# Kernel optimization log

Hardware: AMD Instinct MI355X
Metric: run time of the kernel (lower is better)

Reference implementation:

```python
import jax, jax.numpy as jnp
import numpy as np

B, H, OH, C, T = 512, 1024, 4096, 512, 40


def setup_inputs() -> dict:
    key = jax.random.key(0)
    ks = jax.random.split(key, 5)
    scaled = lambda k, sh, fan: (jax.random.normal(k, sh, jnp.float32) / np.sqrt(fan).astype(np.float32))
    return dict(
        z=jax.random.normal(ks[0], (B, H), jnp.float32),
        timestamps=jnp.arange(T, dtype=jnp.float32) * 0.1,  # spacing == rk4 step_size
        W1=scaled(ks[1], (H, OH), H), b1=jnp.zeros((OH,), jnp.float32),
        W2=scaled(ks[2], (OH, H), OH), b2=jnp.zeros((H,), jnp.float32),
        Wf=scaled(ks[3], (H, C), H), bf=jnp.zeros((C,), jnp.float32),
    )


def reference(z, timestamps, W1, b1, W2, b2, Wf, bf):
    # odefunc: autonomous neural-ODE MLP f(y) = tanh(y W1 + b1) W2 + b2
    def f(y):
        return jnp.tanh(y @ W1 + b1) @ W2 + b2

    # torchdiffeq 'rk4' = 3/8-rule RK4 (rk4_alt_step_func); one step per
    # timestamp interval since spacing == step_size == 0.1
    def step(y, ts):
        t0, t1 = ts
        dt = t1 - t0
        k1 = f(y)
        k2 = f(y + dt * k1 / 3.0)
        k3 = f(y + dt * (k2 - k1 / 3.0))
        k4 = f(y + dt * (k1 - k2 + k3))
        y_new = y + dt * (k1 + 3.0 * (k2 + k3) + k4) / 8.0
        return y_new, y_new

    _, ys = jax.lax.scan(step, z, (timestamps[:-1], timestamps[1:]))
    pred_z = jnp.concatenate([z[None], ys], axis=0)  # [T, B, H], includes y0
    return jax.nn.softmax(pred_z @ Wf + bf, axis=-1)  # [T, B, C]
```

## Files before the change

### kernel.cpp

```cpp
#include <hip/hip_runtime.h>
#include <hip/hip_bf16.h>
#include <math.h>

using bf16 = __hip_bfloat16;
typedef __bf16 bf16x8 __attribute__((ext_vector_type(8)));
typedef float f32x4 __attribute__((ext_vector_type(4)));

static constexpr int NB = 512, NH = 1024, NOH = 4096, NC = 512, NT = 40;
static constexpr int SPLITK = 4;
static constexpr int NCNT = 128;

#define AL(p) __hip_atomic_load((p), __ATOMIC_RELAXED, __HIP_MEMORY_SCOPE_AGENT)
#define ASF(p, v) __hip_atomic_store((p), (v), __ATOMIC_RELAXED, __HIP_MEMORY_SCOPE_AGENT)
#define AFA(p, v) __hip_atomic_fetch_add((p), (v), __ATOMIC_RELAXED, __HIP_MEMORY_SCOPE_AGENT)

__device__ __forceinline__ float lo32f(unsigned long long v) {
  return __uint_as_float((unsigned)v);
}
__device__ __forceinline__ float hi32f(unsigned long long v) {
  return __uint_as_float((unsigned)(v >> 32));
}


__global__ void transpose_cast(const float* __restrict__ W, bf16* __restrict__ WT,
                               int K, int N) {
  __shared__ float tile[32][33];
  const int n0 = blockIdx.x * 32;
  const int k0 = blockIdx.y * 32;
  const int tx = threadIdx.x;
  const int ty = threadIdx.y;
#pragma unroll
  for (int i = 0; i < 4; ++i) {
    int r = ty + i * 8;
    tile[r][tx] = W[(size_t)(k0 + r) * N + n0 + tx];
  }
  __syncthreads();
#pragma unroll
  for (int i = 0; i < 4; ++i) {
    int r = ty + i * 8;
    const int n = n0 + r, k = k0 + tx;
    WT[(size_t)n * K + (k ^ ((n & 7) << 3))] = __float2bfloat16(tile[tx][r]);
  }
}

__global__ void init_state(const float* __restrict__ z, float* __restrict__ y,
                           bf16* __restrict__ yb, bf16* __restrict__ pred0,
                           unsigned* __restrict__ cnt) {
  const int i = blockIdx.x * 256 + threadIdx.x;
  const int r = i >> 10, c = i & (NH - 1);
  float v = z[i];
  y[i] = v;
  bf16 b = __float2bfloat16(v);
  const int sw = r * NH + (c ^ ((r & 7) << 3));
  yb[sw] = b;
  pred0[sw] = b;
  if (i < (NT - 1) * 4 * NCNT) cnt[i] = 0u;
}

template <int EPI>
__global__ __launch_bounds__(256, 3) void gemm_stage(
    const bf16* __restrict__ A, const bf16* __restrict__ BT,
    const float* __restrict__ bias, bf16* __restrict__ outB,
    float* __restrict__ part, float* __restrict__ y, bf16* __restrict__ yb,
    float* __restrict__ k1, float* __restrict__ k2, float* __restrict__ k3,
    bf16* __restrict__ pred_next, const float* __restrict__ ts, int t, int s,
    unsigned* __restrict__ cnt) {
  constexpr int BK = 64;
  constexpr int KCH = 1024;
  constexpr int KST = (EPI == 0) ? NH : NOH;
  constexpr int NOUT = (EPI == 0) ? NOH : NH;
  constexpr int NI = KCH / BK;

  __shared__ __align__(16) bf16 As[3][64 * BK];
  __shared__ __align__(16) bf16 Bs[3][64 * BK];

  const int tid = threadIdx.x;
  const int lane = tid & 63;
  const int wave = tid >> 6;
  const int wr = wave >> 1, wc = wave & 1;
  const int l15 = lane & 15, kg = lane >> 4;
  const int xorB = (l15 & 7) << 4;
  const int srow = tid >> 3;
  const int scol = (tid & 7) * 8;

  const int bid = blockIdx.x;
  const int xcd = bid & 7, slot = bid >> 3;
  int row0, col0, kbeg, kz = 0, strip = 0, rb = 0;
  if constexpr (EPI == 0) {
    col0 = (xcd + ((slot & 7) << 3)) * 64;
    row0 = (slot >> 3) * 64;
    kbeg = 0;
  } else {
    strip = xcd + ((slot & 1) << 3);
    col0 = strip * 64;
    kz = (slot >> 1) & 3;
    rb = slot >> 3;
    row0 = rb * 64;
    kbeg = kz * KCH;
  }

  f32x4 acc[2][2] = {};

  auto stage = [&](int buf, int kt) {
#pragma unroll
    for (int i = 0; i < 2; ++i) {
      const bf16* ga = A + (size_t)(row0 + i * 32 + srow) * KST + kt + scol;
      __builtin_amdgcn_global_load_lds(
          (const __attribute__((address_space(1))) void*)ga,
          (__attribute__((address_space(3))) void*)&As[buf][i * 2048 + tid * 8],
          16, 0, 0);
      const bf16* gb = BT + (size_t)(col0 + i * 32 + srow) * KST + kt + scol;
      __builtin_amdgcn_global_load_lds(
          (const __attribute__((address_space(1))) void*)gb,
          (__attribute__((address_space(3))) void*)&Bs[buf][i * 2048 + tid * 8],
          16, 0, 0);
    }
  };

  stage(0, kbeg);
  stage(1, kbeg + BK);
  int cur = 0, nxt = 2;

#pragma unroll 1
  for (int j = 0; j < NI; ++j) {
    if (j < NI - 1) asm volatile("s_waitcnt vmcnt(4)" ::: "memory");
    else            asm volatile("s_waitcnt vmcnt(0)" ::: "memory");
    __builtin_amdgcn_s_barrier();
    __builtin_amdgcn_sched_barrier(0);
    if (j + 2 < NI) stage(nxt, kbeg + (j + 2) * BK);
    __builtin_amdgcn_sched_barrier(0);

    const char* Ab = (const char*)&As[cur][0];
    const char* Bb = (const char*)&Bs[cur][0];
#pragma unroll
    for (int ks = 0; ks < BK; ks += 32) {
      const int kb2 = (ks + kg * 8) * 2;
      bf16x8 af[2], bf_[2];
#pragma unroll
      for (int mi = 0; mi < 2; ++mi) {
        const int r = wr * 32 + mi * 16 + l15;
        af[mi] = *reinterpret_cast<const bf16x8*>(Ab + ((r * 128 + kb2) ^ xorB));
      }
#pragma unroll
      for (int ni = 0; ni < 2; ++ni) {
        const int r = wc * 32 + ni * 16 + l15;
        bf_[ni] = *reinterpret_cast<const bf16x8*>(Bb + ((r * 128 + kb2) ^ xorB));
      }
#pragma unroll
      for (int mi = 0; mi < 2; ++mi)
#pragma unroll
        for (int ni = 0; ni < 2; ++ni)
          acc[mi][ni] = __builtin_amdgcn_mfma_f32_16x16x32_bf16(
              af[mi], bf_[ni], acc[mi][ni], 0, 0, 0);
    }
    cur = (cur == 2) ? 0 : cur + 1;
    nxt = (nxt == 2) ? 0 : nxt + 1;
  }

  if constexpr (EPI == 0) {
#pragma unroll
    for (int mi = 0; mi < 2; ++mi) {
      const int gr0 = row0 + wr * 32 + mi * 16 + kg * 4;
#pragma unroll
      for (int ni = 0; ni < 2; ++ni) {
        const int gcol = col0 + wc * 32 + ni * 16 + l15;
        const float b = bias[gcol];
#pragma unroll
        for (int j = 0; j < 4; ++j) {
          const int r = gr0 + j;
          outB[(size_t)r * NOUT + (gcol ^ ((r & 7) << 3))] =
              __float2bfloat16(tanhf(acc[mi][ni][j] + b));
        }
      }
    }
  } else {
    float* pz = part + (size_t)kz * (NB * NH);
#pragma unroll
    for (int mi = 0; mi < 2; ++mi) {
      const int gr0 = row0 + wr * 32 + mi * 16 + kg * 4;
#pragma unroll
      for (int ni = 0; ni < 2; ++ni) {
        const int gcol = col0 + wc * 32 + ni * 16 + l15;
#pragma unroll
        for (int j = 0; j < 4; ++j)
          ASF(&pz[(size_t)(gr0 + j) * NH + gcol], acc[mi][ni][j]);
      }
    }
    __syncthreads();
    __shared__ unsigned arrS;
    if (tid == 0) arrS = AFA(&cnt[rb * 16 + strip], 1u);
    __syncthreads();
    if (arrS == (unsigned)(SPLITK - 1)) {
      const float dtv = ts[t + 1] - ts[t];
#pragma unroll
      for (int q = 0; q < 4; ++q) {
        const int v = q * 256 + tid;
        const int r = v >> 4, c4 = v & 15;
        const int row = row0 + r, col = col0 + c4 * 4;
        const size_t gi = (size_t)row * NH + col;
        f32x4 sum = {};
#pragma unroll
        for (int z = 0; z < SPLITK; ++z) {
          const unsigned long long* pp =
              (const unsigned long long*)(part + (size_t)z * (NB * NH) + gi);
          unsigned long long u0 = AL(pp), u1 = AL(pp + 1);
          sum[0] += lo32f(u0); sum[1] += hi32f(u0);
          sum[2] += lo32f(u1); sum[3] += hi32f(u1);
        }
        const f32x4 bb = *reinterpret_cast<const f32x4*>(bias + col);
        const f32x4 ksv = sum + bb;
        const f32x4 yv = *reinterpret_cast<const f32x4*>(y + gi);
        f32x4 yn;
        if (s == 1) {
          *reinterpret_cast<f32x4*>(k1 + gi) = ksv;
          yn = yv + ksv * (dtv / 3.0f);
        } else if (s == 2) {
          const f32x4 k1v = *reinterpret_cast<const f32x4*>(k1 + gi);
          *reinterpret_cast<f32x4*>(k2 + gi) = ksv;
          yn = yv + (ksv - k1v * (1.0f / 3.0f)) * dtv;
        } else if (s == 3) {
          const f32x4 k1v = *reinterpret_cast<const f32x4*>(k1 + gi);
          const f32x4 k2v = *reinterpret_cast<const f32x4*>(k2 + gi);
          *reinterpret_cast<f32x4*>(k3 + gi) = ksv;
          yn = yv + (k1v - k2v + ksv) * dtv;
        } else {
          const f32x4 k1v = *reinterpret_cast<const f32x4*>(k1 + gi);
          const f32x4 k2v = *reinterpret_cast<const f32x4*>(k2 + gi);
          const f32x4 k3v = *reinterpret_cast<const f32x4*>(k3 + gi);
          yn = yv + (k1v + (k2v + k3v) * 3.0f + ksv) * (dtv * 0.125f);
          *reinterpret_cast<f32x4*>(y + gi) = yn;
        }
        union { bf16 h4[4]; unsigned long long u; } pk;
#pragma unroll
        for (int j = 0; j < 4; ++j) pk.h4[j] = __float2bfloat16(yn[j]);
        const size_t sw =
            (size_t)row * NH + (((col & ~7) ^ ((row & 7) << 3)) | (col & 7));
        *reinterpret_cast<unsigned long long*>(yb + sw) = pk.u;
        if (s == 4)
          *reinterpret_cast<unsigned long long*>(pred_next + sw) = pk.u;
      }
    }
  }
}

__global__ __launch_bounds__(256, 1) void proj_gemm(
    const bf16* __restrict__ A, const bf16* __restrict__ BT,
    int M, int N, int K, const float* __restrict__ bias,
    float* __restrict__ outF) {
  __shared__ __align__(16) bf16 As[2][128 * 64];
  __shared__ __align__(16) bf16 Bs[2][128 * 64];

  const int tid = threadIdx.x;
  const int lane = tid & 63;
  const int wave = tid >> 6;
  const int wr = wave >> 1, wc = wave & 1;
  const int row0 = blockIdx.y * 128, col0 = blockIdx.x * 128;
  const int l15 = lane & 15, kg = lane >> 4;
  const int xorB = (l15 & 7) << 4;
  const int srow = tid >> 3;
  const int scol = (tid & 7) * 8;

  f32x4 acc[4][4] = {};

  auto stage = [&](int buf, int kt) {
#pragma unroll
    for (int i = 0; i < 4; ++i) {
      const bf16* ga = A + (size_t)(row0 + i * 32 + srow) * K + kt + scol;
      __builtin_amdgcn_global_load_lds(
          (const __attribute__((address_space(1))) void*)ga,
          (__attribute__((address_space(3))) void*)&As[buf][i * 2048 + tid * 8],
          16, 0, 0);
      const bf16* gb = BT + (size_t)(col0 + i * 32 + srow) * K + kt + scol;
      __builtin_amdgcn_global_load_lds(
          (const __attribute__((address_space(1))) void*)gb,
          (__attribute__((address_space(3))) void*)&Bs[buf][i * 2048 + tid * 8],
          16, 0, 0);
    }
  };

  stage(0, 0);
  __syncthreads();
  int cur = 0;

  for (int kt = 0; kt < K; kt += 64) {
    if (kt + 64 < K) stage(cur ^ 1, kt + 64);
#pragma unroll
    for (int ks = 0; ks < 64; ks += 32) {
      const int kb2 = (ks + kg * 8) * 2;
      bf16x8 af[4], bf_[4];
#pragma unroll
      for (int mi = 0; mi < 4; ++mi) {
        const int r = wr * 64 + mi * 16 + l15;
        af[mi] = *reinterpret_cast<const bf16x8*>(
            (const char*)&As[cur][0] + ((r * 128 + kb2) ^ xorB));
      }
#pragma unroll
      for (int ni = 0; ni < 4; ++ni) {
        const int r = wc * 64 + ni * 16 + l15;
        bf_[ni] = *reinterpret_cast<const bf16x8*>(
            (const char*)&Bs[cur][0] + ((r * 128 + kb2) ^ xorB));
      }
#pragma unroll
      for (int mi = 0; mi < 4; ++mi)
#pragma unroll
        for (int ni = 0; ni < 4; ++ni)
          acc[mi][ni] = __builtin_amdgcn_mfma_f32_16x16x32_bf16(
              af[mi], bf_[ni], acc[mi][ni], 0, 0, 0);
    }
    __syncthreads();
    cur ^= 1;
  }

#pragma unroll
  for (int mi = 0; mi < 4; ++mi) {
    const int gr0 = row0 + wr * 64 + mi * 16 + kg * 4;
#pragma unroll
    for (int ni = 0; ni < 4; ++ni) {
      const int gcol = col0 + wc * 64 + ni * 16 + l15;
      const float b = bias[gcol];
#pragma unroll
      for (int j = 0; j < 4; ++j)
        outF[(size_t)(gr0 + j) * N + gcol] = acc[mi][ni][j] + b;
    }
  }
}

__global__ void softmax_rows(float* __restrict__ out) {
  const int row = blockIdx.x * 4 + (threadIdx.x >> 6);
  const int lane = threadIdx.x & 63;
  float* p = out + (size_t)row * NC + lane * 8;
  f32x4 a = *reinterpret_cast<const f32x4*>(p);
  f32x4 b = *reinterpret_cast<const f32x4*>(p + 4);

  float m = fmaxf(fmaxf(fmaxf(a[0], a[1]), fmaxf(a[2], a[3])),
                  fmaxf(fmaxf(b[0], b[1]), fmaxf(b[2], b[3])));
#pragma unroll
  for (int off = 32; off > 0; off >>= 1) m = fmaxf(m, __shfl_xor(m, off));

  f32x4 ea, eb;
  float sum = 0.0f;
#pragma unroll
  for (int j = 0; j < 4; ++j) { ea[j] = expf(a[j] - m); sum += ea[j]; }
#pragma unroll
  for (int j = 0; j < 4; ++j) { eb[j] = expf(b[j] - m); sum += eb[j]; }
#pragma unroll
  for (int off = 32; off > 0; off >>= 1) sum += __shfl_xor(sum, off);

  const float inv = 1.0f / sum;
  ea *= inv;
  eb *= inv;
  *reinterpret_cast<f32x4*>(p) = ea;
  *reinterpret_cast<f32x4*>(p + 4) = eb;
}

extern "C" void kernel_launch(void* const* d_in, const int* in_sizes, int n_in,
                              void* d_out, int out_size, void* d_ws, size_t ws_size,
                              hipStream_t stream) {
  const float* z = (const float*)d_in[0];
  const float* ts = (const float*)d_in[1];
  const float* W1 = (const float*)d_in[2];
  const float* b1 = (const float*)d_in[3];
  const float* W2 = (const float*)d_in[4];
  const float* b2 = (const float*)d_in[5];
  const float* Wf = (const float*)d_in[6];
  const float* bfv = (const float*)d_in[7];

  char* w = (char*)d_ws;
  bf16* W1bT = (bf16*)w;          w += (size_t)NOH * NH * 2;
  bf16* W2bT = (bf16*)w;          w += (size_t)NH * NOH * 2;
  bf16* WfT  = (bf16*)w;          w += (size_t)NC * NH * 2;
  float* y   = (float*)w;         w += (size_t)NB * NH * 4;
  bf16* yb   = (bf16*)w;          w += (size_t)NB * NH * 2;
  float* k1  = (float*)w;         w += (size_t)NB * NH * 4;
  float* k2  = (float*)w;         w += (size_t)NB * NH * 4;
  float* k3  = (float*)w;         w += (size_t)NB * NH * 4;
  bf16* h    = (bf16*)w;          w += (size_t)NB * NOH * 2;
  float* part = (float*)w;        w += (size_t)SPLITK * NB * NH * 4;
  bf16* pred = (bf16*)w;          w += (size_t)NT * NB * NH * 2;
  unsigned* cnt = (unsigned*)w;   w += (size_t)(NT - 1) * 4 * NCNT * 4;

  float* logits = (float*)d_out;

  transpose_cast<<<dim3(NOH / 32, NH / 32), dim3(32, 8), 0, stream>>>(W1, W1bT, NH, NOH);
  transpose_cast<<<dim3(NH / 32, NOH / 32), dim3(32, 8), 0, stream>>>(W2, W2bT, NOH, NH);
  transpose_cast<<<dim3(NC / 32, NH / 32), dim3(32, 8), 0, stream>>>(Wf, WfT, NH, NC);
  init_state<<<(NB * NH) / 256, 256, 0, stream>>>(z, y, yb, pred, cnt);

  for (int t = 0; t < NT - 1; ++t) {
    for (int s = 1; s <= 4; ++s) {
      gemm_stage<0><<<512, 256, 0, stream>>>(
          yb, W1bT, b1, h, nullptr, nullptr, nullptr, nullptr, nullptr,
          nullptr, nullptr, ts, t, s, nullptr);
      gemm_stage<1><<<512, 256, 0, stream>>>(
          h, W2bT, b2, nullptr, part, y, yb, k1, k2, k3,
          pred + (size_t)(t + 1) * NB * NH, ts, t, s,
          cnt + (size_t)(t * 4 + (s - 1)) * NCNT);
    }
  }

  proj_gemm<<<dim3(NC / 128, (NT * NB) / 128), 256, 0, stream>>>(
      pred, WfT, NT * NB, NC, NH, bfv, logits);
  softmax_rows<<<(NT * NB) / 4, 256, 0, stream>>>(logits);
}
```

Before: 5.071 ms.

## Deepen GEMM LDS pipeline, co-locate split-K blocks per XCD, drop atomic partial stores

The GEMM main loop moves from three to four LDS buffers and prefetches three K-tiles ahead, with waitcnt thresholds adjusted to match. Occupancy is lowered to two blocks per CU to make room for the larger shared memory. The split-K block mapping is reordered so the four K-chunks of a tile share one XCD and its L2. Partial sums are now written and read with plain vector accesses, guarded by an acquire load on the arrival counter, instead of per-element atomics. This trades occupancy and a weaker memory-ordering pattern for more load latency hiding and cheaper reduction traffic.

```diff
diff --git a/kernel.cpp b/kernel.cpp
--- a/kernel.cpp
+++ b/kernel.cpp
@@ -10,16 +10,8 @@
 static constexpr int SPLITK = 4;
 static constexpr int NCNT = 128;
 
-#define AL(p) __hip_atomic_load((p), __ATOMIC_RELAXED, __HIP_MEMORY_SCOPE_AGENT)
-#define ASF(p, v) __hip_atomic_store((p), (v), __ATOMIC_RELAXED, __HIP_MEMORY_SCOPE_AGENT)
-#define AFA(p, v) __hip_atomic_fetch_add((p), (v), __ATOMIC_RELAXED, __HIP_MEMORY_SCOPE_AGENT)
-
-__device__ __forceinline__ float lo32f(unsigned long long v) {
-  return __uint_as_float((unsigned)v);
-}
-__device__ __forceinline__ float hi32f(unsigned long long v) {
-  return __uint_as_float((unsigned)(v >> 32));
-}
+#define AFA_RLX(p, v) __hip_atomic_fetch_add((p), (v), __ATOMIC_RELAXED, __HIP_MEMORY_SCOPE_AGENT)
+#define AL_ACQ(p) __hip_atomic_load((p), __ATOMIC_ACQUIRE, __HIP_MEMORY_SCOPE_AGENT)
 
 
 __global__ void transpose_cast(const float* __restrict__ W, bf16* __restrict__ WT,
@@ -58,7 +50,7 @@
 }
 
 template <int EPI>
-__global__ __launch_bounds__(256, 3) void gemm_stage(
+__global__ __launch_bounds__(256, 2) void gemm_stage(
     const bf16* __restrict__ A, const bf16* __restrict__ BT,
     const float* __restrict__ bias, bf16* __restrict__ outB,
     float* __restrict__ part, float* __restrict__ y, bf16* __restrict__ yb,
@@ -71,8 +63,8 @@
   constexpr int NOUT = (EPI == 0) ? NOH : NH;
   constexpr int NI = KCH / BK;
 
-  __shared__ __align__(16) bf16 As[3][64 * BK];
-  __shared__ __align__(16) bf16 Bs[3][64 * BK];
+  __shared__ __align__(16) bf16 As[4][64 * BK];
+  __shared__ __align__(16) bf16 Bs[4][64 * BK];
 
   const int tid = threadIdx.x;
   const int lane = tid & 63;
@@ -85,18 +77,20 @@
 
   const int bid = blockIdx.x;
   const int xcd = bid & 7, slot = bid >> 3;
-  int row0, col0, kbeg, kz = 0, strip = 0, rb = 0;
+  int row0, col0, kbeg, kz = 0, tileId = 0;
   if constexpr (EPI == 0) {
     col0 = (xcd + ((slot & 7) << 3)) * 64;
     row0 = (slot >> 3) * 64;
     kbeg = 0;
   } else {
-    strip = xcd + ((slot & 1) << 3);
+    kz = slot & 3;
+    const int local = slot >> 2;
+    const int strip = xcd * 2 + (local & 1);
+    const int rb = local >> 1;
     col0 = strip * 64;
-    kz = (slot >> 1) & 3;
-    rb = slot >> 3;
     row0 = rb * 64;
     kbeg = kz * KCH;
+    tileId = strip * 8 + rb;
   }
 
   f32x4 acc[2][2] = {};
@@ -119,19 +113,19 @@
 
   stage(0, kbeg);
   stage(1, kbeg + BK);
-  int cur = 0, nxt = 2;
+  stage(2, kbeg + 2 * BK);
 
 #pragma unroll 1
   for (int j = 0; j < NI; ++j) {
-    if (j < NI - 1) asm volatile("s_waitcnt vmcnt(4)" ::: "memory");
-    else            asm volatile("s_waitcnt vmcnt(0)" ::: "memory");
+    if (j < NI - 2)       asm volatile("s_waitcnt vmcnt(8)" ::: "memory");
+    else if (j == NI - 2) asm volatile("s_waitcnt vmcnt(4)" ::: "memory");
+    else                  asm volatile("s_waitcnt vmcnt(0)" ::: "memory");
     __builtin_amdgcn_s_barrier();
     __builtin_amdgcn_sched_barrier(0);
-    if (j + 2 < NI) stage(nxt, kbeg + (j + 2) * BK);
-    __builtin_amdgcn_sched_barrier(0);
-
-    const char* Ab = (const char*)&As[cur][0];
-    const char* Bb = (const char*)&Bs[cur][0];
+    if (j + 3 < NI) stage((j + 3) & 3, kbeg + (j + 3) * BK);
+
+    const char* Ab = (const char*)&As[j & 3][0];
+    const char* Bb = (const char*)&Bs[j & 3][0];
 #pragma unroll
     for (int ks = 0; ks < BK; ks += 32) {
       const int kb2 = (ks + kg * 8) * 2;
@@ -153,8 +147,6 @@
           acc[mi][ni] = __builtin_amdgcn_mfma_f32_16x16x32_bf16(
               af[mi], bf_[ni], acc[mi][ni], 0, 0, 0);
     }
-    cur = (cur == 2) ? 0 : cur + 1;
-    nxt = (nxt == 2) ? 0 : nxt + 1;
   }
 
   if constexpr (EPI == 0) {
@@ -183,14 +175,15 @@
         const int gcol = col0 + wc * 32 + ni * 16 + l15;
 #pragma unroll
         for (int j = 0; j < 4; ++j)
-          ASF(&pz[(size_t)(gr0 + j) * NH + gcol], acc[mi][ni][j]);
+          pz[(size_t)(gr0 + j) * NOUT + gcol] = acc[mi][ni][j];
       }
     }
     __syncthreads();
     __shared__ unsigned arrS;
-    if (tid == 0) arrS = AFA(&cnt[rb * 16 + strip], 1u);
+    if (tid == 0) arrS = AFA_RLX(&cnt[tileId], 1u);
     __syncthreads();
     if (arrS == (unsigned)(SPLITK - 1)) {
+      (void)AL_ACQ(&cnt[tileId]);
       const float dtv = ts[t + 1] - ts[t];
 #pragma unroll
       for (int q = 0; q < 4; ++q) {
@@ -200,13 +193,8 @@
         const size_t gi = (size_t)row * NH + col;
         f32x4 sum = {};
 #pragma unroll
-        for (int z = 0; z < SPLITK; ++z) {
-          const unsigned long long* pp =
-              (const unsigned long long*)(part + (size_t)z * (NB * NH) + gi);
-          unsigned long long u0 = AL(pp), u1 = AL(pp + 1);
-          sum[0] += lo32f(u0); sum[1] += hi32f(u0);
-          sum[2] += lo32f(u1); sum[3] += hi32f(u1);
-        }
+        for (int z = 0; z < SPLITK; ++z)
+          sum += *reinterpret_cast<const f32x4*>(part + (size_t)z * (NB * NH) + gi);
         const f32x4 bb = *reinterpret_cast<const f32x4*>(bias + col);
         const f32x4 ksv = sum + bb;
         const f32x4 yv = *reinterpret_cast<const f32x4*>(y + gi);
```

After: 5.721 ms. +12.8%, slower.
